# Optimization experiments

Measured on AMD Instinct MI355X. Metric: run time of the kernel, lower is better.

## Reference

```python
import jax, jax.numpy as jnp
import numpy as np

D_MODEL = 768
NUM_HEADS = 12
HEAD_DIM = D_MODEL // NUM_HEADS


def setup_inputs() -> dict:
    key = jax.random.key(0)
    ks = jax.random.split(key, 9)
    B, S = 2, 2048
    s = 1.0 / np.sqrt(D_MODEL)
    x = jax.random.normal(ks[0], (B, S, D_MODEL), dtype=jnp.float32)
    Wq = jax.random.normal(ks[1], (D_MODEL, D_MODEL), dtype=jnp.float32) * s
    Wk = jax.random.normal(ks[2], (D_MODEL, D_MODEL), dtype=jnp.float32) * s
    Wv = jax.random.normal(ks[3], (D_MODEL, D_MODEL), dtype=jnp.float32) * s
    Wo = jax.random.normal(ks[4], (D_MODEL, D_MODEL), dtype=jnp.float32) * s
    bq = jax.random.normal(ks[5], (D_MODEL,), dtype=jnp.float32) * 0.01
    bk = jax.random.normal(ks[6], (D_MODEL,), dtype=jnp.float32) * 0.01
    bv = jax.random.normal(ks[7], (D_MODEL,), dtype=jnp.float32) * 0.01
    bo = jax.random.normal(ks[8], (D_MODEL,), dtype=jnp.float32) * 0.01
    return {"x": x, "Wq": Wq, "bq": bq, "Wk": Wk, "bk": bk,
            "Wv": Wv, "bv": bv, "Wo": Wo, "bo": bo}


def reference(x, Wq, bq, Wk, bk, Wv, bv, Wo, bo):
    B, S, _ = x.shape
    # projections; reshape to [B, H, S, Dh]
    def split_heads(t):
        return t.reshape(B, S, NUM_HEADS, HEAD_DIM).transpose(0, 2, 1, 3)
    q = split_heads(x @ Wq + bq)
    k = split_heads(x @ Wk + bk)
    v = split_heads(x @ Wv + bv)
    scale = 1.0 / np.sqrt(HEAD_DIM)
    scores = jnp.einsum("bhqd,bhkd->bhqk", q, k) * scale  # [B,H,S,S]
    attn = jax.nn.softmax(scores, axis=-1)
    # dropout p=0.0 (eval) -> identity
    ctx = jnp.einsum("bhqk,bhkd->bhqd", attn, v)
    ctx = ctx.transpose(0, 2, 1, 3).reshape(B, S, D_MODEL)
    return ctx @ Wo + bo
```

## Files before the change

### kernel.cpp

```cpp
#include <hip/hip_runtime.h>
#include <hip/hip_bf16.h>
#include <hip/hip_fp16.h>

#define D_MODEL 768
#define NHEADS  12
#define HD      64
#define BATCH   2
#define SEQ     2048
#define NTOK    (BATCH*SEQ)
#define NX      ((size_t)NTOK * D_MODEL)
#define NW      ((size_t)D_MODEL * D_MODEL)
#define NBH     (BATCH*NHEADS)
#define SC_LOG2 0.18033688f

typedef __attribute__((ext_vector_type(8))) short    short8;
typedef __attribute__((ext_vector_type(8))) _Float16 half8;
typedef __attribute__((ext_vector_type(2))) __fp16   fp16x2;
typedef __attribute__((ext_vector_type(4))) float    f32x4;

__device__ __forceinline__ float bf2f(short s) {
    union { unsigned u; float f; } c;
    c.u = ((unsigned)(unsigned short)s) << 16;
    return c.f;
}
__device__ __forceinline__ short f2bf(float f) {
    __hip_bfloat16 h = __float2bfloat16(f);
    return *(short*)&h;
}

#ifdef __has_builtin
#if __has_builtin(__builtin_amdgcn_global_load_lds)
#define HAS_GLD 1
#endif
#if __has_builtin(__builtin_amdgcn_exp2f)
#define EXP2(x) __builtin_amdgcn_exp2f(x)
#else
#define EXP2(x) exp2f(x)
#endif
#if __has_builtin(__builtin_amdgcn_cvt_pkrtz)
#define HAS_PKRTZ 1
#endif
#else
#define EXP2(x) exp2f(x)
#endif
#ifdef HAS_GLD
#define GLD16(gp, lp) __builtin_amdgcn_global_load_lds( \
    (const __attribute__((address_space(1))) void*)(gp), \
    (__attribute__((address_space(3))) void*)(lp), 16, 0, 0)
#endif

#ifdef HAS_PKRTZ
#define PKF16(a, b) __builtin_amdgcn_cvt_pkrtz((a), (b))
#else
#define PKF16(a, b) ((fp16x2){ (__fp16)(a), (__fp16)(b) })
#endif

__global__ __launch_bounds__(256) void fused_conv(
        const void* __restrict__ xin,
        const void* __restrict__ w0, const void* __restrict__ w1,
        const void* __restrict__ w2, const void* __restrict__ w3,
        const void* __restrict__ b0, const void* __restrict__ b1,
        const void* __restrict__ b2, const void* __restrict__ b3,
        short* __restrict__ xc, short* __restrict__ wt,
        short* __restrict__ bc, int* __restrict__ flag)
{
    __shared__ int red[256];
    __shared__ float T[64][65];
    const int tid = threadIdx.x;
    const int F = blockIdx.x;

    {
        const short* xs = (const short*)xin;
        int maxe = 0;
#pragma unroll
        for (int u = 0; u < 16; ++u) {
            int e = ((unsigned short)xs[tid * 16 + u] >> 7) & 0xFF;
            maxe = max(maxe, e);
        }
        red[tid] = maxe;
        __syncthreads();
        for (int s = 128; s > 0; s >>= 1) {
            if (tid < s) red[tid] = max(red[tid], red[tid + s]);
            __syncthreads();
        }
    }
    const bool isf = (red[0] > 140);

    if (F < 3072) {
        const int i = F * 256 + tid;
        if (isf) {
            float4 f = ((const float4*)xin)[i];
            short4 o = { f2bf(f.x), f2bf(f.y), f2bf(f.z), f2bf(f.w) };
            ((short4*)xc)[i] = o;
        } else {
            ((short4*)xc)[i] = ((const short4*)xin)[i];
        }
    } else if (F < 3648) {
        const int G = F - 3072;
        const int z = G / 144, rr = G % 144;
        const int k0 = (rr % 12) * 64, n0 = (rr / 12) * 64;
        const void* src = (z == 0) ? w0 : (z == 1) ? w1 : (z == 2) ? w2 : w3;
        const float sc = (z == 0) ? SC_LOG2 : 1.0f;
        const int la = tid & 15, lb = tid >> 4;
#pragma unroll
        for (int u = 0; u < 4; ++u) {
            const int kr = (lb & 3) + 4 * u + 16 * (lb >> 2);
            if (isf) {
                float4 f = *(const float4*)((const float*)src + (size_t)(k0 + kr) * D_MODEL + n0 + la * 4);
                T[kr][la*4+0] = f.x; T[kr][la*4+1] = f.y; T[kr][la*4+2] = f.z; T[kr][la*4+3] = f.w;
            } else {
                short4 s = *(const short4*)((const short*)src + (size_t)(k0 + kr) * D_MODEL + n0 + la * 4);
                T[kr][la*4+0] = bf2f(s.x); T[kr][la*4+1] = bf2f(s.y);
                T[kr][la*4+2] = bf2f(s.z); T[kr][la*4+3] = bf2f(s.w);
            }
        }
        __syncthreads();
#pragma unroll
        for (int u = 0; u < 4; ++u) {
            const int nr = (lb & 3) + 4 * u + 16 * (lb >> 2);
            short4 o = { f2bf(T[la*4+0][nr] * sc), f2bf(T[la*4+1][nr] * sc),
                         f2bf(T[la*4+2][nr] * sc), f2bf(T[la*4+3][nr] * sc) };
            *(short4*)(wt + (size_t)z * NW + (size_t)(n0 + nr) * D_MODEL + k0 + la * 4) = o;
        }
    } else {
        if (tid == 0) *flag = isf ? 1 : 0;
        const void* srcs[4] = { b0, b1, b2, b3 };
        for (int z = 0; z < 4; ++z) {
            const float sc = (z == 0) ? SC_LOG2 : 1.0f;
            for (int i = tid; i < D_MODEL; i += 256) {
                float v = isf ? ((const float*)srcs[z])[i] : bf2f(((const short*)srcs[z])[i]);
                bc[z * D_MODEL + i] = f2bf(v * sc);
            }
        }
    }
}

__global__ __launch_bounds__(512) void qkv_gemm(const short* __restrict__ X,
                                                const short* __restrict__ Wt,
                                                const short* __restrict__ bias,
                                                short* __restrict__ qb,
                                                short* __restrict__ kb,
                                                _Float16* __restrict__ Vt)
{
    __shared__ __align__(16) char shbuf[32768];
    short* Als = (short*)shbuf;
    short* Bls = (short*)(shbuf + 16384);
    _Float16* T = (_Float16*)shbuf;

    const int tid = threadIdx.x;
    const int wave = tid >> 6, lane = tid & 63;
    const int quad = lane >> 4, l16 = lane & 15;
    const int wm = wave & 3, wn = wave >> 2;
    const int m0 = blockIdx.x * 128;
    const int ng = blockIdx.y * 128;

    f32x4 acc[2][4];
#pragma unroll
    for (int nt = 0; nt < 4; ++nt) {
        const float bv = bf2f(bias[ng + wn*64 + nt*16 + l16]);
#pragma unroll
        for (int mt = 0; mt < 2; ++mt) acc[mt][nt] = (f32x4){bv, bv, bv, bv};
    }

    const int row = tid >> 2, ch = (tid & 3) * 8;
#ifdef HAS_GLD
#define QSTAGE(buf, k0) do { \
        GLD16(X  + (size_t)(m0 + row) * D_MODEL + (k0) + ch, &Als[(buf)*4096 + tid*8]); \
        GLD16(Wt + (size_t)(ng + row) * D_MODEL + (k0) + ch, &Bls[(buf)*4096 + tid*8]); \
    } while (0)
#else
#define QSTAGE(buf, k0) do { \
        short8 r0 = *(const short8*)(X  + (size_t)(m0 + row) * D_MODEL + (k0) + ch); \
        short8 r1 = *(const short8*)(Wt + (size_t)(ng + row) * D_MODEL + (k0) + ch); \
        *(short8*)&Als[(buf)*4096 + tid*8] = r0; \
        *(short8*)&Bls[(buf)*4096 + tid*8] = r1; \
    } while (0)
#endif

    QSTAGE(0, 0);
    __syncthreads();

    for (int ks = 0; ks < 24; ++ks) {
        const int cur = ks & 1;
        if (ks + 1 < 24) QSTAGE(cur ^ 1, (ks + 1) * 32);

        short8 a[2], b[4];
#pragma unroll
        for (int mt = 0; mt < 2; ++mt)
            a[mt] = *(const short8*)&Als[cur*4096 + (wm*32 + mt*16 + l16) * 32 + quad*8];
#pragma unroll
        for (int nt = 0; nt < 4; ++nt)
            b[nt] = *(const short8*)&Bls[cur*4096 + (wn*64 + nt*16 + l16) * 32 + quad*8];
#pragma unroll
        for (int mt = 0; mt < 2; ++mt)
#pragma unroll
        for (int nt = 0; nt < 4; ++nt)
            acc[mt][nt] = __builtin_amdgcn_mfma_f32_16x16x32_bf16(a[mt], b[nt], acc[mt][nt], 0, 0, 0);

        __syncthreads();
    }
#undef QSTAGE

    const int seg = blockIdx.y / 6;
    if (seg < 2) {
        short* out = seg ? kb : qb;
        const int nl = ng - seg * 768;
#pragma unroll
        for (int mt = 0; mt < 2; ++mt)
#pragma unroll
        for (int nt = 0; nt < 4; ++nt) {
            const int n = nl + wn*64 + nt*16 + l16;
#pragma unroll
            for (int r = 0; r < 4; ++r) {
                const int m = m0 + wm*32 + mt*16 + quad*4 + r;
                out[(size_t)m * D_MODEL + n] = f2bf(acc[mt][nt][r]);
            }
        }
    } else {
        const int batch = m0 >> 11, tokb0 = m0 & (SEQ - 1);
#pragma unroll
        for (int p = 0; p < 2; ++p) {
            if ((wm >> 1) == p) {
#pragma unroll
                for (int nt = 0; nt < 4; ++nt) {
                    const int dim_l = wn*64 + nt*16 + l16;
#pragma unroll
                    for (int mt = 0; mt < 2; ++mt) {
                        const int tok_l = (wm & 1)*32 + mt*16 + quad*4;
                        union { _Float16 h4[4]; int2 v; } u;
#pragma unroll
                        for (int r = 0; r < 4; ++r) u.h4[r] = (_Float16)acc[mt][nt][r];
                        *(int2*)&T[dim_l * 72 + tok_l] = u.v;
                    }
                }
            }
            __syncthreads();
#pragma unroll
            for (int u = 0; u < 2; ++u) {
                const int slot = tid + u * 512;
                const int drow = slot >> 3, chk = slot & 7;
                int4 val = *(const int4*)&T[drow * 72 + chk * 8];
                const int dim_g = ng - 1536 + drow;
                const int h = dim_g >> 6, d = dim_g & 63;
                *(int4*)(Vt + ((size_t)(batch * NHEADS + h) * HD + d) * SEQ
                              + tokb0 + p*64 + chk*8) = val;
            }
            if (p == 0) __syncthreads();
        }
    }
}

__global__ __launch_bounds__(256) void out_gemm(const _Float16* __restrict__ Op,
                                                const float* __restrict__ mlp,
                                                const short* __restrict__ Wt,
                                                const short* __restrict__ bias,
                                                void* __restrict__ outv,
                                                const int* __restrict__ flag)
{
    __shared__ short Als[2][2048];
    __shared__ short Bls[2][2048];

    const int tid = threadIdx.x;
    const int wave = tid >> 6, lane = tid & 63;
    const int quad = lane >> 4, l16 = lane & 15;
    const int m0 = blockIdx.x * 64;
    const int n0 = blockIdx.y * 64;

    f32x4 acc[4];
#pragma unroll
    for (int nt = 0; nt < 4; ++nt) {
        const float bv = bf2f(bias[n0 + nt*16 + l16]);
        acc[nt] = (f32x4){bv, bv, bv, bv};
    }

    const int row = tid >> 2, ch = (tid & 3) * 8;
    const int m = m0 + row;
    const int bhb = (m >> 11) * NHEADS;
    const int qq = m & (SEQ - 1);
    const _Float16* Op2 = Op + (size_t)(NBH * SEQ) * HD;

#define XLOAD(ks) do { \
        const int cc = (ks) * 32 + ch; \
        const int h = cc >> 6, d = cc & 63; \
        const size_t r1 = (size_t)(bhb + h) * SEQ + qq; \
        const float2 ml1 = *(const float2*)&mlp[r1 * 2]; \
        const float2 ml2 = *(const float2*)&mlp[((size_t)(NBH * SEQ) + r1) * 2]; \
        p1 = *(const half8*)&Op[r1 * HD + d]; \
        p2 = *(const half8*)&Op2[r1 * HD + d]; \
        const float M_ = fmaxf(ml1.x, ml2.x); \
        const float w1 = EXP2(ml1.x - M_) * ml1.y; \
        const float w2 = EXP2(ml2.x - M_) * ml2.y; \
        const float s_ = 1.0f / (w1 + w2); \
        f1 = w1 * s_; f2 = w2 * s_; \
    } while (0)

#define XSTORE(buf) do { \
        short8 xb; \
        _Pragma("unroll") \
        for (int j = 0; j < 8; ++j) \
            xb[j] = f2bf(f1 * (float)p1[j] + f2 * (float)p2[j]); \
        *(short8*)&Als[buf][tid*8] = xb; \
    } while (0)

#ifdef HAS_GLD
#define BSTAGE(buf, k0) \
        GLD16(Wt + (size_t)(n0 + row) * D_MODEL + (k0) + ch, &Bls[buf][tid*8])
#else
#define BSTAGE(buf, k0) do { \
        short8 r1_ = *(const short8*)(Wt + (size_t)(n0 + row) * D_MODEL + (k0) + ch); \
        *(short8*)&Bls[buf][tid*8] = r1_; } while (0)
#endif

    half8 p1, p2; float f1, f2;
    XLOAD(0); XSTORE(0);
    BSTAGE(0, 0);
    __syncthreads();

    for (int ks = 0; ks < 24; ++ks) {
        const int cur = ks & 1;
        if (ks + 1 < 24) {
            XLOAD(ks + 1);
            BSTAGE(cur ^ 1, (ks + 1) * 32);
        }

        short8 a = *(const short8*)&Als[cur][(wave*16 + l16) * 32 + quad*8];
#pragma unroll
        for (int nt = 0; nt < 4; ++nt) {
            short8 b = *(const short8*)&Bls[cur][(nt*16 + l16) * 32 + quad*8];
            acc[nt] = __builtin_amdgcn_mfma_f32_16x16x32_bf16(a, b, acc[nt], 0, 0, 0);
        }

        if (ks + 1 < 24) XSTORE(cur ^ 1);
        __syncthreads();
    }
#undef XLOAD
#undef XSTORE
#undef BSTAGE

    const bool outf32 = (*flag != 0);
#pragma unroll
    for (int nt = 0; nt < 4; ++nt) {
        const int n = n0 + nt*16 + l16;
#pragma unroll
        for (int r = 0; r < 4; ++r) {
            const int mm = m0 + wave*16 + quad*4 + r;
            const size_t idx = (size_t)mm * D_MODEL + n;
            if (outf32) ((float*)outv)[idx] = acc[nt][r];
            else        ((short*)outv)[idx] = f2bf(acc[nt][r]);
        }
    }
}

__global__ __launch_bounds__(256, 3) void attn_mfma(const short* __restrict__ q,
                                                    const short* __restrict__ k,
                                                    const _Float16* __restrict__ Vt,
                                                    _Float16* __restrict__ Op,
                                                    float* __restrict__ mlp)
{
    __shared__ __align__(16) short    Kls[2][4096];
    __shared__ __align__(16) _Float16 Vls[2][4096];
    __shared__ __align__(16) _Float16 Pls[4][2048];

    const int tid  = threadIdx.x;
    const int wave = tid >> 6, lane = tid & 63;
    const int quad = lane >> 4, l16 = lane & 15;

    const int F = blockIdx.x;
    const int xcd = F & 7, slot = F >> 3;
    const int bh = xcd * 3 + (slot >> 5);
    const int rem = slot & 31;
    const int q0 = (rem >> 1) * 128;
    const int sp = rem & 1;
    const int kb0 = sp * (SEQ / 2);
    const int b = bh / NHEADS, h = bh % NHEADS;
    const size_t bS = (size_t)b * SEQ;

    short8 qf[2][2];
#pragma unroll
    for (int col = 0; col < 2; ++col)
#pragma unroll
    for (int k0h = 0; k0h < 2; ++k0h)
        qf[col][k0h] = *(const short8*)(q + (bS + q0 + wave*32 + col*16 + l16) * D_MODEL
                                          + h*HD + k0h*32 + quad*8);

    half8 ones;
#pragma unroll
    for (int j = 0; j < 8; ++j) ones[j] = (_Float16)1.0f;

    const int cK0 = tid >> 6,         keyK0 = tid & 63;
    const int cK1 = (tid + 256) >> 6, keyK1 = tid & 63;
    const short* kgp0 = k + (bS + kb0 + keyK0) * D_MODEL + h*HD + cK0*8;
    const short* kgp1 = k + (bS + kb0 + keyK1) * D_MODEL + h*HD + cK1*8;
    const _Float16* vgp0 = Vt + ((size_t)bh * HD + keyK0) * SEQ + kb0 + cK0*8;
    const _Float16* vgp1 = Vt + ((size_t)bh * HD + keyK1) * SEQ + kb0 + cK1*8;

#ifdef HAS_GLD
#define STAGE_K(buf, j0) do { \
        GLD16(kgp0 + (size_t)(j0) * D_MODEL, &Kls[buf][tid*8]); \
        GLD16(kgp1 + (size_t)(j0) * D_MODEL, &Kls[buf][(tid+256)*8]); \
    } while (0)
#define STAGE_V(buf, j0) do { \
        GLD16(vgp0 + (j0), &Vls[buf][tid*8]); \
        GLD16(vgp1 + (j0), &Vls[buf][(tid+256)*8]); \
    } while (0)
#else
#define STAGE_K(buf, j0) do { \
        short8 a_ = *(const short8*)(kgp0 + (size_t)(j0) * D_MODEL); \
        short8 b_ = *(const short8*)(kgp1 + (size_t)(j0) * D_MODEL); \
        *(short8*)&Kls[buf][tid*8] = a_;  *(short8*)&Kls[buf][(tid+256)*8] = b_; \
    } while (0)
#define STAGE_V(buf, j0) do { \
        half8 c_ = *(const half8*)(vgp0 + (j0)); \
        half8 d_ = *(const half8*)(vgp1 + (j0)); \
        *(half8*)&Vls[buf][tid*8] = c_;  *(half8*)&Vls[buf][(tid+256)*8] = d_; \
    } while (0)
#endif

    float m_ = -1e30f;
    f32x4 laccA = (f32x4){0.f,0.f,0.f,0.f}, laccB = (f32x4){0.f,0.f,0.f,0.f};
    f32x4 o[4][2];
#pragma unroll
    for (int t = 0; t < 4; ++t) { o[t][0] = (f32x4){0.f,0.f,0.f,0.f}; o[t][1] = (f32x4){0.f,0.f,0.f,0.f}; }

#define NT (SEQ / 2 / 64)

#define QK(S, KB) do { \
    _Pragma("unroll") \
    for (int t = 0; t < 4; ++t) { S[t][0] = (f32x4){0.f,0.f,0.f,0.f}; S[t][1] = (f32x4){0.f,0.f,0.f,0.f}; } \
    _Pragma("unroll") \
    for (int k0h = 0; k0h < 2; ++k0h) \
    _Pragma("unroll") \
    for (int t = 0; t < 4; ++t) { \
        short8 kf = *(const short8*)&Kls[KB][(k0h*4 + quad)*512 + (t*16 + l16)*8]; \
        S[t][0] = __builtin_amdgcn_mfma_f32_16x16x32_bf16(kf, qf[0][k0h], S[t][0], 0, 0, 0); \
        S[t][1] = __builtin_amdgcn_mfma_f32_16x16x32_bf16(kf, qf[1][k0h], S[t][1], 0, 0, 0); \
    } \
} while (0)

#define PV(VB) do { \
    _Pragma("unroll") \
    for (int k0h = 0; k0h < 2; ++k0h) { \
        half8 pf0 = *(half8*)&Pls[wave][(k0h*4 + quad)*128 + l16*8]; \
        half8 pf1 = *(half8*)&Pls[wave][1024 + (k0h*4 + quad)*128 + l16*8]; \
        laccA = __builtin_amdgcn_mfma_f32_16x16x32_f16(ones, pf0, laccA, 0, 0, 0); \
        laccB = __builtin_amdgcn_mfma_f32_16x16x32_f16(ones, pf1, laccB, 0, 0, 0); \
        _Pragma("unroll") \
        for (int t = 0; t < 4; ++t) { \
            half8 vf = *(const half8*)&Vls[VB][(k0h*4 + quad)*512 + (t*16 + l16)*8]; \
            o[t][0] = __builtin_amdgcn_mfma_f32_16x16x32_f16(vf, pf0, o[t][0], 0, 0, 0); \
            o[t][1] = __builtin_amdgcn_mfma_f32_16x16x32_f16(vf, pf1, o[t][1], 0, 0, 0); \
        } \
    } \
} while (0)

#define SOFTMAX(S) do { \
    float mx = S[0][0][0]; \
    _Pragma("unroll") \
    for (int t = 0; t < 4; ++t) \
    _Pragma("unroll") \
    for (int c = 0; c < 2; ++c) \
    _Pragma("unroll") \
    for (int r = 0; r < 4; ++r) mx = fmaxf(mx, S[t][c][r]); \
    if (__any(mx > m_ + 8.f)) { \
        _Pragma("unroll") \
        for (int d = 1; d < 64; d <<= 1) mx = fmaxf(mx, __shfl_xor(mx, d)); \
        const float mn = fmaxf(m_, mx); \
        const float al = EXP2(m_ - mn); \
        _Pragma("unroll") \
        for (int t = 0; t < 4; ++t) \
        _Pragma("unroll") \
        for (int c = 0; c < 2; ++c) { \
            o[t][c][0] *= al; o[t][c][1] *= al; o[t][c][2] *= al; o[t][c][3] *= al; \
        } \
        laccA[0] *= al; laccB[0] *= al; \
        m_ = mn; \
    } \
    _Pragma("unroll") \
    for (int t = 0; t < 4; ++t) \
    _Pragma("unroll") \
    for (int c = 0; c < 2; ++c) { \
        union { fp16x2 h2[2]; int2 v; } u4; \
        u4.h2[0] = PKF16(EXP2(S[t][c][0] - m_), EXP2(S[t][c][1] - m_)); \
        u4.h2[1] = PKF16(EXP2(S[t][c][2] - m_), EXP2(S[t][c][3] - m_)); \
        const int kc = 2*t + (quad >> 1); \
        *(int2*)&Pls[wave][c*1024 + kc*128 + l16*8 + (quad & 1)*4] = u4.v; \
    } \
} while (0)

#define BODY(JT) do { \
    if ((JT) + 2 < NT) STAGE_K(((JT) + 2) & 1, ((JT) + 2) * 64); \
    if ((JT) + 1 < NT) STAGE_V(((JT) + 1) & 1, ((JT) + 1) * 64); \
    f32x4 s_[4][2]; \
    __builtin_amdgcn_s_setprio(1); \
    if ((JT) + 1 < NT) QK(s_, ((JT) + 1) & 1); \
    PV((JT) & 1); \
    __builtin_amdgcn_s_setprio(0); \
    if ((JT) + 1 < NT) SOFTMAX(s_); \
    __syncthreads(); \
} while (0)

    STAGE_K(0, 0); STAGE_V(0, 0);
    __syncthreads();
    STAGE_K(1, 64);
    {
        f32x4 s_[4][2];
        QK(s_, 0);
        SOFTMAX(s_);
    }
    __syncthreads();

    for (int jt = 0; jt < NT; ++jt) BODY(jt);

#pragma unroll
    for (int col = 0; col < 2; ++col) {
        const f32x4 la = col ? laccB : laccA;
        const float inv = 1.0f / la[0];
        const int myq = q0 + wave*32 + col*16 + l16;
        const size_t prow = ((size_t)sp * (NBH * SEQ) + (size_t)bh * SEQ + myq);
        _Float16* orow = Op + prow * HD;
#pragma unroll
        for (int t = 0; t < 4; ++t) {
            union { _Float16 h4[4]; int2 v; } u4;
#pragma unroll
            for (int r = 0; r < 4; ++r) u4.h4[r] = (_Float16)(o[t][col][r] * inv);
            *(int2*)(orow + t*16 + quad*4) = u4.v;
        }
        if (quad == 0) {
            float2 mlv; mlv.x = m_; mlv.y = la[0];
            *(float2*)&mlp[prow * 2] = mlv;
        }
    }
#undef BODY
#undef SOFTMAX
#undef PV
#undef QK
#undef NT
#undef STAGE_K
#undef STAGE_V
}

extern "C" void kernel_launch(void* const* d_in, const int* in_sizes, int n_in,
                              void* d_out, int out_size, void* d_ws, size_t ws_size,
                              hipStream_t stream)
{
    int* flag = (int*)d_ws;
    short* xc = (short*)((char*)d_ws + 64);
    short* Wt = xc + NX;
    short* bc = Wt + 4 * NW;
    short* qb = bc + 4 * D_MODEL;
    short* kb = qb + NX;
    _Float16* Vt = (_Float16*)(kb + NX);
    _Float16* Op = (_Float16*)(Vt + NX);
    float* mlp = (float*)(Op + (size_t)2 * NBH * SEQ * HD);

    fused_conv<<<3649, 256, 0, stream>>>(d_in[0],
                                         d_in[1], d_in[3], d_in[5], d_in[7],
                                         d_in[2], d_in[4], d_in[6], d_in[8],
                                         xc, Wt, bc, flag);

    qkv_gemm<<<dim3(NTOK/128, 2304/128), 512, 0, stream>>>(xc, Wt, bc, qb, kb, Vt);

    attn_mfma<<<768, 256, 0, stream>>>(qb, kb, Vt, Op, mlp);

    out_gemm<<<dim3(NTOK/64, D_MODEL/64), 256, 0, stream>>>(Op, mlp, Wt + 3*NW, bc + 3*D_MODEL, d_out, flag);
}
```

Measured before the change: 169.8 us.

## Store K and V in tile-contiguous layout matching attention LDS staging

The QKV projection epilogue now writes K and V into a pre-tiled layout. In that layout each 64-key tile per head is a contiguous 4096-element block, ordered exactly as the attention kernel's shared-memory staging expects. The attention kernel then loads each tile with fully contiguous 16-byte reads instead of strided row gathers across D_MODEL or SEQ. This improves global load coalescing in the attention hot loop. In exchange, the K epilogue uses scattered 2-byte stores and the V transpose write pattern changes.

```diff
diff --git a/kernel.cpp b/kernel.cpp
--- a/kernel.cpp
+++ b/kernel.cpp
@@ -202,18 +202,33 @@
 #undef QSTAGE
 
     const int seg = blockIdx.y / 6;
-    if (seg < 2) {
-        short* out = seg ? kb : qb;
-        const int nl = ng - seg * 768;
+    if (seg == 0) {
+#pragma unroll
+        for (int mt = 0; mt < 2; ++mt)
+#pragma unroll
+        for (int nt = 0; nt < 4; ++nt) {
+            const int n = ng + wn*64 + nt*16 + l16;
+#pragma unroll
+            for (int r = 0; r < 4; ++r) {
+                const int m = m0 + wm*32 + mt*16 + quad*4 + r;
+                qb[(size_t)m * D_MODEL + n] = f2bf(acc[mt][nt][r]);
+            }
+        }
+    } else if (seg == 1) {
+        const int nl = ng - 768;
 #pragma unroll
         for (int mt = 0; mt < 2; ++mt)
 #pragma unroll
         for (int nt = 0; nt < 4; ++nt) {
             const int n = nl + wn*64 + nt*16 + l16;
+            const int h = n >> 6, dh = n & 63;
+            const int chunk = dh >> 3, dof = dh & 7;
 #pragma unroll
             for (int r = 0; r < 4; ++r) {
                 const int m = m0 + wm*32 + mt*16 + quad*4 + r;
-                out[(size_t)m * D_MODEL + n] = f2bf(acc[mt][nt][r]);
+                const int b2 = m >> 11, tok = m & (SEQ - 1);
+                kb[((size_t)(b2*NHEADS + h)*32 + (tok >> 6))*4096
+                   + chunk*512 + (tok & 63)*8 + dof] = f2bf(acc[mt][nt][r]);
             }
         }
     } else {
@@ -238,12 +253,12 @@
 #pragma unroll
             for (int u = 0; u < 2; ++u) {
                 const int slot = tid + u * 512;
-                const int drow = slot >> 3, chk = slot & 7;
+                const int drow = slot & 127, chk = slot >> 7;
                 int4 val = *(const int4*)&T[drow * 72 + chk * 8];
                 const int dim_g = ng - 1536 + drow;
-                const int h = dim_g >> 6, d = dim_g & 63;
-                *(int4*)(Vt + ((size_t)(batch * NHEADS + h) * HD + d) * SEQ
-                              + tokb0 + p*64 + chk*8) = val;
+                const int h = dim_g >> 6, dl = dim_g & 63;
+                *(int4*)(Vt + ((size_t)((batch*NHEADS + h)*32) + (tokb0 >> 6) + p)*4096
+                            + chk*512 + dl*8) = val;
             }
             if (p == 0) __syncthreads();
         }
@@ -371,7 +386,6 @@
     const int rem = slot & 31;
     const int q0 = (rem >> 1) * 128;
     const int sp = rem & 1;
-    const int kb0 = sp * (SEQ / 2);
     const int b = bh / NHEADS, h = bh % NHEADS;
     const size_t bS = (size_t)b * SEQ;
 
@@ -387,31 +401,27 @@
 #pragma unroll
     for (int j = 0; j < 8; ++j) ones[j] = (_Float16)1.0f;
 
-    const int cK0 = tid >> 6,         keyK0 = tid & 63;
-    const int cK1 = (tid + 256) >> 6, keyK1 = tid & 63;
-    const short* kgp0 = k + (bS + kb0 + keyK0) * D_MODEL + h*HD + cK0*8;
-    const short* kgp1 = k + (bS + kb0 + keyK1) * D_MODEL + h*HD + cK1*8;
-    const _Float16* vgp0 = Vt + ((size_t)bh * HD + keyK0) * SEQ + kb0 + cK0*8;
-    const _Float16* vgp1 = Vt + ((size_t)bh * HD + keyK1) * SEQ + kb0 + cK1*8;
+    const short*    kbase = k  + ((size_t)bh*32 + sp*16) * 4096;
+    const _Float16* vbase = Vt + ((size_t)bh*32 + sp*16) * 4096;
 
 #ifdef HAS_GLD
 #define STAGE_K(buf, j0) do { \
-        GLD16(kgp0 + (size_t)(j0) * D_MODEL, &Kls[buf][tid*8]); \
-        GLD16(kgp1 + (size_t)(j0) * D_MODEL, &Kls[buf][(tid+256)*8]); \
+        GLD16(kbase + (size_t)(j0)*64 + tid*8,       &Kls[buf][tid*8]); \
+        GLD16(kbase + (size_t)(j0)*64 + (tid+256)*8, &Kls[buf][(tid+256)*8]); \
     } while (0)
 #define STAGE_V(buf, j0) do { \
-        GLD16(vgp0 + (j0), &Vls[buf][tid*8]); \
-        GLD16(vgp1 + (j0), &Vls[buf][(tid+256)*8]); \
+        GLD16(vbase + (size_t)(j0)*64 + tid*8,       &Vls[buf][tid*8]); \
+        GLD16(vbase + (size_t)(j0)*64 + (tid+256)*8, &Vls[buf][(tid+256)*8]); \
     } while (0)
 #else
 #define STAGE_K(buf, j0) do { \
-        short8 a_ = *(const short8*)(kgp0 + (size_t)(j0) * D_MODEL); \
-        short8 b_ = *(const short8*)(kgp1 + (size_t)(j0) * D_MODEL); \
+        short8 a_ = *(const short8*)(kbase + (size_t)(j0)*64 + tid*8); \
+        short8 b_ = *(const short8*)(kbase + (size_t)(j0)*64 + (tid+256)*8); \
         *(short8*)&Kls[buf][tid*8] = a_;  *(short8*)&Kls[buf][(tid+256)*8] = b_; \
     } while (0)
 #define STAGE_V(buf, j0) do { \
-        half8 c_ = *(const half8*)(vgp0 + (j0)); \
-        half8 d_ = *(const half8*)(vgp1 + (j0)); \
+        half8 c_ = *(const half8*)(vbase + (size_t)(j0)*64 + tid*8); \
+        half8 d_ = *(const half8*)(vbase + (size_t)(j0)*64 + (tid+256)*8); \
         *(half8*)&Vls[buf][tid*8] = c_;  *(half8*)&Vls[buf][(tid+256)*8] = d_; \
     } while (0)
 #endif
```

Measured after the change: 166.2 us. 2.1% less time.
